# Kernel tuning notes

Hardware: AMD Instinct MI355X
Metric: run time of the kernel (lower is better)

## Reference

```python
import jax, jax.numpy as jnp
import numpy as np

N, E, C, R = 50000, 800000, 64, 8
H = 64  # MLP hidden width


def setup_inputs() -> dict:
    key = jax.random.key(0)
    ks = jax.random.split(key, 11)
    return {
        "node_features": jax.random.normal(ks[0], (N, 4 * C), jnp.float32),  # [0e: C] ++ [1o: C*3]
        "sph_harmonics": jax.random.normal(ks[1], (E, 4), jnp.float32),      # [Y_00, Y_1m (3)]
        "radial_basis": jax.random.normal(ks[2], (E, R), jnp.float32),
        "pre_W0": jax.random.normal(ks[3], (C, C), jnp.float32),
        "pre_W1": jax.random.normal(ks[4], (C, C), jnp.float32),
        "mlp_W1": jax.random.normal(ks[5], (R, H), jnp.float32) / np.sqrt(R),
        "mlp_W2": jax.random.normal(ks[6], (H, H), jnp.float32) / np.sqrt(H),
        "mlp_W3": jax.random.normal(ks[7], (H, 4 * C), jnp.float32) / np.sqrt(H),
        "post_W0": jax.random.normal(ks[8], (C, C), jnp.float32),
        "post_W1": jax.random.normal(ks[9], (C, C), jnp.float32),
        "edge_index": jax.random.randint(ks[10], (2, E), 0, N),  # row 0: receiver, row 1: sender
    }


def reference(node_features, sph_harmonics, radial_basis,
              pre_W0, pre_W1, mlp_W1, mlp_W2, mlp_W3, post_W0, post_W1,
              edge_index):
    n = node_features.shape[0]
    c = pre_W0.shape[0]
    inv_sqrt_c = 1.0 / jnp.sqrt(jnp.asarray(c, jnp.float32))
    INV_SQRT2 = 0.7071067811865476   # path normalization (2 paths per output irrep)
    INV_SQRT3 = 0.5773502691896258   # CG norm for 1o x 1o -> 0e (dot)

    # split flattened irreps: scalars [n, c], vectors [n, c, 3]
    x0 = node_features[:, :c]
    x1 = node_features[:, c:].reshape(n, c, 3)

    # pre_linear: per-irrep channel mixing (e3nn o3.Linear with 1/sqrt(fan_in))
    x0 = (x0 @ pre_W0) * inv_sqrt_c
    x1 = jnp.einsum('ncm,cd->ndm', x1, pre_W1) * inv_sqrt_c

    recv, send = edge_index[0], edge_index[1]

    # gather neighbour features (irregular access)
    xj0 = x0[send]            # [E, c]
    xj1 = x1[send]            # [E, c, 3]
    sh0 = sph_harmonics[:, :1]  # [E, 1]
    sh1 = sph_harmonics[:, 1:]  # [E, 3]

    # per-edge generated tensor-product weights: SiLU MLP, no bias, linear last layer
    h = jax.nn.silu(radial_basis @ mlp_W1)
    h = jax.nn.silu(h @ mlp_W2)
    w = h @ mlp_W3            # [E, 4c]
    w00, w110, w01, w10 = w[:, :c], w[:, c:2 * c], w[:, 2 * c:3 * c], w[:, 3 * c:]

    # channelwise CG tensor product with per-edge weights
    # 0e outputs: (0e x 0e) and (1o . 1o)/sqrt(3)
    m0 = (w00 * xj0 * sh0 + w110 * (jnp.einsum('ecm,em->ec', xj1, sh1) * INV_SQRT3)) * INV_SQRT2
    # 1o outputs: (0e x 1o) and (1o x 0e)
    m1 = (w01[:, :, None] * xj0[:, :, None] * sh1[:, None, :]
          + w10[:, :, None] * xj1 * sh0[:, :, None]) * INV_SQRT2   # [E, c, 3]

    # scatter-reduce (sum aggregation) into receiving nodes
    agg0 = jax.ops.segment_sum(m0, recv, num_segments=n)           # [n, c]
    agg1 = jax.ops.segment_sum(m1, recv, num_segments=n)           # [n, c, 3]

    # post_linear: per-irrep channel mixing
    y0 = (agg0 @ post_W0) * inv_sqrt_c
    y1 = jnp.einsum('ncm,cd->ndm', agg1, post_W1) * inv_sqrt_c

    # UnflattenIrreps -> [n, channels, sum(2l+1)] = [n, c, 4]
    return jnp.concatenate([y0[:, :, None], y1], axis=-1)
```

## Files before the change

kernel.cpp:

```cpp
#include <hip/hip_runtime.h>


#define FDIM 256
#define INV_SQRT2 0.7071067811865476f
#define INV_SQRT3 0.5773502691896258f

typedef __attribute__((ext_vector_type(8))) short s16x8;
typedef __attribute__((ext_vector_type(4))) float fx4;

__device__ __forceinline__ float silu_f(float x) { return x / (1.0f + __expf(-x)); }

__device__ __forceinline__ unsigned short f2bf(float x) {
    unsigned int u = __float_as_uint(x);
    u += 0x7FFFu + ((u >> 16) & 1u);
    return (unsigned short)(u >> 16);
}

__device__ __forceinline__ float bf2f(short v) {
    return __uint_as_float(((unsigned int)(unsigned short)v) << 16);
}

__device__ __forceinline__ int swz(int row) {
    return ((row & 7) ^ ((row >> 3) & 7)) << 4;
}

__global__ void __launch_bounds__(256) hist_pre_kernel(
    const int* __restrict__ ei, int* __restrict__ cnt, int E,
    const float* __restrict__ W1, const float* __restrict__ W2,
    const float* __restrict__ W3, float* __restrict__ W1t,
    unsigned short* __restrict__ W2bf, unsigned short* __restrict__ W3bf,
    const float* __restrict__ nf, const float* __restrict__ preW0,
    const float* __restrict__ preW1, unsigned short* __restrict__ xtb,
    int nNodes)
{
    int i = blockIdx.x * 256 + threadIdx.x;
    if (i < 512)  { int r = i >> 6, k = i & 63; W1t[k * 8 + r] = W1[i]; }
    if (i < 4096) { int j = i >> 6, k = i & 63; W2bf[i] = f2bf(W2[k * 64 + j]); }
    if (i < 16384) {
        int col = i >> 6, k = i & 63;
        int cb = col >> 5, r32 = col & 31, t = r32 >> 3, ci = r32 & 7;
        W3bf[i] = f2bf(W3[k * 256 + t * 64 + cb * 8 + ci]);
    }
    if (i < E) atomicAdd(&cnt[ei[i]], 1);

    const int lane = threadIdx.x & 63;
    const int wave = threadIdx.x >> 6;
    const int waveId = blockIdx.x * 4 + wave;
    const int nWaves = gridDim.x * 4;

    __shared__ __align__(16) float rowL[4][2][256];

    float w0r[64], w1r[64];
#pragma unroll
    for (int c = 0; c < 64; ++c) {
        w0r[c] = preW0[c * 64 + lane];
        w1r[c] = preW1[c * 64 + lane];
    }

    int n = waveId;
    if (n < nNodes) {
        float4 rv = *reinterpret_cast<const float4*>(nf + (size_t)n * FDIM + lane * 4);
        *reinterpret_cast<float4*>(&rowL[wave][0][lane * 4]) = rv;
    }
    int buf = 0;
    for (; n < nNodes; n += nWaves, buf ^= 1) {
        const int nn = n + nWaves;
        const bool hasNext = (nn < nNodes);
        float4 rvn;
        if (hasNext)
            rvn = *reinterpret_cast<const float4*>(nf + (size_t)nn * FDIM + lane * 4);

        asm volatile("s_waitcnt lgkmcnt(0)" ::: "memory");
        __builtin_amdgcn_sched_barrier(0);

        const float* __restrict__ row = rowL[wave][buf];
        float a0 = 0.f, a1 = 0.f, a2 = 0.f, a3 = 0.f;
#pragma unroll
        for (int c4 = 0; c4 < 16; ++c4) {
            fx4 x0 = *reinterpret_cast<const fx4*>(&row[c4 * 4]);
            fx4 xa = *reinterpret_cast<const fx4*>(&row[64 + c4 * 12]);
            fx4 xb = *reinterpret_cast<const fx4*>(&row[64 + c4 * 12 + 4]);
            fx4 xc = *reinterpret_cast<const fx4*>(&row[64 + c4 * 12 + 8]);
            const int c = c4 * 4;
            a0 = fmaf(x0[0], w0r[c + 0], a0);
            a1 = fmaf(xa[0], w1r[c + 0], a1);
            a2 = fmaf(xa[1], w1r[c + 0], a2);
            a3 = fmaf(xa[2], w1r[c + 0], a3);
            a0 = fmaf(x0[1], w0r[c + 1], a0);
            a1 = fmaf(xa[3], w1r[c + 1], a1);
            a2 = fmaf(xb[0], w1r[c + 1], a2);
            a3 = fmaf(xb[1], w1r[c + 1], a3);
            a0 = fmaf(x0[2], w0r[c + 2], a0);
            a1 = fmaf(xb[2], w1r[c + 2], a1);
            a2 = fmaf(xb[3], w1r[c + 2], a2);
            a3 = fmaf(xc[0], w1r[c + 2], a3);
            a0 = fmaf(x0[3], w0r[c + 3], a0);
            a1 = fmaf(xc[1], w1r[c + 3], a1);
            a2 = fmaf(xc[2], w1r[c + 3], a2);
            a3 = fmaf(xc[3], w1r[c + 3], a3);
        }
        __builtin_amdgcn_sched_barrier(0);

        unsigned short* o = xtb + (size_t)n * FDIM + (lane >> 3) * 32 + (lane & 7);
        o[0]  = f2bf(a0 * 0.125f);
        o[8]  = f2bf(a1 * 0.125f);
        o[16] = f2bf(a2 * 0.125f);
        o[24] = f2bf(a3 * 0.125f);

        if (hasNext)
            *reinterpret_cast<float4*>(&rowL[wave][buf ^ 1][lane * 4]) = rvn;
        __builtin_amdgcn_sched_barrier(0);
    }
}

__global__ void __launch_bounds__(1024) scan_kernel(
    const int* __restrict__ cnt, int* __restrict__ cursor, int nBins)
{
    __shared__ int part[1024];
    const int t = threadIdx.x;
    const int per = (nBins + 1023) / 1024;
    const int lo = t * per;
    const int hi = (lo + per < nBins) ? lo + per : nBins;

    int s = 0;
    for (int i = lo; i < hi; ++i) s += cnt[i];
    part[t] = s;
    __syncthreads();

    for (int off = 1; off < 1024; off <<= 1) {
        int v = part[t];
        int add = (t >= off) ? part[t - off] : 0;
        __syncthreads();
        part[t] = v + add;
        __syncthreads();
    }

    int run = part[t] - s;
    for (int i = lo; i < hi; ++i) {
        cursor[i] = run;
        run += cnt[i];
    }
}

__global__ void __launch_bounds__(256) scatter_perm_kernel(
    const int* __restrict__ ei, int* __restrict__ cursor,
    int* __restrict__ perm, int2* __restrict__ ers, int E)
{
    int i = blockIdx.x * 256 + threadIdx.x;
    if (i < E) {
        int r = ei[i];
        int p = atomicAdd(&cursor[r], 1);
        perm[p] = i;
        ers[p] = make_int2(r, ei[E + i]);
    }
}

__global__ void __launch_bounds__(256, 2) edge_kernel(
    const unsigned short* __restrict__ xtb, const float* __restrict__ sph,
    const float* __restrict__ rb, const int2* __restrict__ ers,
    const int* __restrict__ perm,
    const float* __restrict__ W1t, const unsigned short* __restrict__ W2bf,
    const unsigned short* __restrict__ W3bf, float* __restrict__ agg, int E)
{
    const int tid  = threadIdx.x;
    const int lane = tid & 63;
    const int wave = tid >> 6;
    const int eBase = blockIdx.x * 256 + wave * 64;
    const int idx = eBase + lane;
    const int idxSafe = (idx < E) ? idx : (E - 1);
    const int pe = perm[idxSafe];

    __shared__ __align__(16) char sbufAll[4][16384];
    __shared__ int recvL[4][64];
    char* const sbuf = sbufAll[wave];

    const float4 rq0 = *reinterpret_cast<const float4*>(rb + (size_t)pe * 8);
    const float4 rq1 = *reinterpret_cast<const float4*>(rb + (size_t)pe * 8 + 4);
    const float rbv[8] = {rq0.x, rq0.y, rq0.z, rq0.w, rq1.x, rq1.y, rq1.z, rq1.w};

    float h1[64];
#pragma unroll
    for (int k = 0; k < 64; ++k) {
        float acc = 0.f;
#pragma unroll
        for (int r = 0; r < 8; ++r) acc = fmaf(rbv[r], W1t[k * 8 + r], acc);
        h1[k] = silu_f(acc);
    }

#pragma unroll
    for (int q = 0; q < 8; ++q) {
        s16x8 v;
#pragma unroll
        for (int t = 0; t < 8; ++t) v[t] = (short)f2bf(h1[q * 8 + t]);
        *reinterpret_cast<s16x8*>(sbuf + lane * 128 + ((q * 16) ^ swz(lane))) = v;
    }

    const float4 shv = *reinterpret_cast<const float4*>(sph + (size_t)pe * 4);
    const float sh1a[3] = {shv.y, shv.z, shv.w};
    const int2 rs = ers[idxSafe];
    recvL[wave][lane] = rs.x;
    const unsigned short* __restrict__ xrow = xtb + (size_t)rs.y * FDIM;

    const int l15 = lane & 15;
    const int g4  = lane >> 4;

    s16x8 aH[4][2];
#pragma unroll
    for (int m = 0; m < 4; ++m)
#pragma unroll
        for (int kk = 0; kk < 2; ++kk) {
            int row = m * 16 + l15;
            aH[m][kk] = *reinterpret_cast<const s16x8*>(
                sbuf + row * 128 + ((kk * 64 + g4 * 16) ^ swz(row)));
        }

#pragma unroll
    for (int nh = 0; nh < 2; ++nh) {
        s16x8 bW2[2][2];
#pragma unroll
        for (int n2 = 0; n2 < 2; ++n2)
#pragma unroll
            for (int kk = 0; kk < 2; ++kk)
                bW2[n2][kk] = *reinterpret_cast<const s16x8*>(
                    W2bf + ((nh * 2 + n2) * 16 + l15) * 64 + kk * 32 + g4 * 8);

        fx4 acc2[4][2];
#pragma unroll
        for (int m = 0; m < 4; ++m)
#pragma unroll
            for (int n2 = 0; n2 < 2; ++n2) {
                fx4 z = {0.f, 0.f, 0.f, 0.f};
                acc2[m][n2] = z;
            }
#pragma unroll
        for (int kk = 0; kk < 2; ++kk)
#pragma unroll
            for (int m = 0; m < 4; ++m)
#pragma unroll
                for (int n2 = 0; n2 < 2; ++n2)
                    acc2[m][n2] = __builtin_amdgcn_mfma_f32_16x16x32_bf16(
                        aH[m][kk], bW2[n2][kk], acc2[m][n2], 0, 0, 0);

#pragma unroll
        for (int m = 0; m < 4; ++m)
#pragma unroll
            for (int n2 = 0; n2 < 2; ++n2)
#pragma unroll
                for (int r = 0; r < 4; ++r) {
                    int edge = m * 16 + g4 * 4 + r;
                    int j = (nh * 2 + n2) * 16 + l15;
                    *reinterpret_cast<unsigned short*>(
                        sbuf + edge * 128 + ((2 * j) ^ swz(edge))) =
                        f2bf(silu_f(acc2[m][n2][r]));
                }
    }

    s16x8 aH2[4][2];
#pragma unroll
    for (int m = 0; m < 4; ++m)
#pragma unroll
        for (int kk = 0; kk < 2; ++kk) {
            int row = m * 16 + l15;
            aH2[m][kk] = *reinterpret_cast<const s16x8*>(
                sbuf + row * 128 + ((kk * 64 + g4 * 16) ^ swz(row)));
        }

    const int jj  = lane & 31;
    const int sub = lane >> 5;
    const int base = sub * 32;
    float* const aggJJ = agg + jj;

    unsigned segmask = 0;
    {
        int rp = recvL[wave][base];
#pragma unroll
        for (int ep = 1; ep < 32; ++ep) {
            int r = recvL[wave][base + ep];
            if (r != rp) segmask |= (1u << ep);
            rp = r;
        }
    }

    for (int cbp = 0; cbp < 4; ++cbp) {
        s16x8 xjb2[8];
#pragma unroll
        for (int t = 0; t < 8; ++t)
            xjb2[t] = *reinterpret_cast<const s16x8*>(xrow + cbp * 64 + t * 8);

#pragma unroll
        for (int half = 0; half < 2; ++half) {
            const int cb = cbp * 2 + half;
            const s16x8* xjb = &xjb2[half * 4];

            s16x8 bW3[2][2];
#pragma unroll
            for (int n2 = 0; n2 < 2; ++n2)
#pragma unroll
                for (int kk = 0; kk < 2; ++kk)
                    bW3[n2][kk] = *reinterpret_cast<const s16x8*>(
                        W3bf + (cb * 32 + n2 * 16 + l15) * 64 + kk * 32 + g4 * 8);

            fx4 accw[4][2];
#pragma unroll
            for (int m = 0; m < 4; ++m)
#pragma unroll
                for (int n2 = 0; n2 < 2; ++n2) {
                    fx4 z = {0.f, 0.f, 0.f, 0.f};
                    accw[m][n2] = z;
                }
#pragma unroll
            for (int kk = 0; kk < 2; ++kk)
#pragma unroll
                for (int m = 0; m < 4; ++m)
#pragma unroll
                    for (int n2 = 0; n2 < 2; ++n2)
                        accw[m][n2] = __builtin_amdgcn_mfma_f32_16x16x32_bf16(
                            aH2[m][kk], bW3[n2][kk], accw[m][n2], 0, 0, 0);

#pragma unroll
            for (int m = 0; m < 4; ++m)
#pragma unroll
                for (int n2 = 0; n2 < 2; ++n2)
#pragma unroll
                    for (int r = 0; r < 4; ++r) {
                        int edge = m * 16 + g4 * 4 + r;
                        int c32 = n2 * 16 + l15;
                        *reinterpret_cast<float*>(
                            sbuf + edge * 128 + ((c32 * 4) ^ swz(edge))) = accw[m][n2][r];
                    }

            float wv[4][8];
#pragma unroll
            for (int t = 0; t < 4; ++t)
#pragma unroll
                for (int q = 0; q < 2; ++q) {
                    fx4 v = *reinterpret_cast<const fx4*>(
                        sbuf + lane * 128 + ((t * 32 + q * 16) ^ swz(lane)));
                    wv[t][q*4+0]=v.x; wv[t][q*4+1]=v.y; wv[t][q*4+2]=v.z; wv[t][q*4+3]=v.w;
                }

#pragma unroll
            for (int ci = 0; ci < 8; ++ci) {
                float x0v = bf2f(xjb[0][ci]);
                float x1a = bf2f(xjb[1][ci]);
                float x1b = bf2f(xjb[2][ci]);
                float x1c = bf2f(xjb[3][ci]);
                float dotv = (x1a * sh1a[0] + x1b * sh1a[1] + x1c * sh1a[2]) * INV_SQRT3;
                float m0 = (wv[0][ci] * x0v * shv.x + wv[1][ci] * dotv) * INV_SQRT2;
                float m1 = (wv[2][ci] * x0v * sh1a[0] + wv[3][ci] * x1a * shv.x) * INV_SQRT2;
                float m2 = (wv[2][ci] * x0v * sh1a[1] + wv[3][ci] * x1b * shv.x) * INV_SQRT2;
                float m3 = (wv[2][ci] * x0v * sh1a[2] + wv[3][ci] * x1c * shv.x) * INV_SQRT2;
                wv[0][ci] = m0; wv[1][ci] = m1; wv[2][ci] = m2; wv[3][ci] = m3;
            }
#pragma unroll
            for (int t = 0; t < 4; ++t)
#pragma unroll
                for (int q = 0; q < 2; ++q) {
                    fx4 v = {wv[t][q*4+0], wv[t][q*4+1], wv[t][q*4+2], wv[t][q*4+3]};
                    *reinterpret_cast<fx4*>(
                        sbuf + lane * 128 + ((t * 32 + q * 16) ^ swz(lane))) = v;
                }

            {
                int rprev = recvL[wave][base];
                float acc = 0.f;
                bool first = true;
#pragma unroll
                for (int ep = 0; ep < 32; ++ep) {
                    const int eL = base + ep;
                    float v = *reinterpret_cast<const float*>(
                        sbuf + eL * 128 + ((jj * 4) ^ swz(eL)));
                    if (eBase + eL >= E) v = 0.f;
                    if (segmask & (1u << ep)) {
                        float* dst = aggJJ + (size_t)rprev * FDIM + cb * 32;
                        if (first) atomicAdd(dst, acc);
                        else       *dst = acc;
                        first = false;
                        acc = 0.f;
                        rprev = recvL[wave][eL];
                    }
                    acc += v;
                }
                atomicAdd(aggJJ + (size_t)rprev * FDIM + cb * 32, acc);
            }
        }
    }
}

__global__ void __launch_bounds__(256) post_kernel(
    const float* __restrict__ agg, const float* __restrict__ W0,
    const float* __restrict__ W1, float* __restrict__ out, int nNodes)
{
    const int lane = threadIdx.x & 63;
    const int wave = threadIdx.x >> 6;
    const int waveId = blockIdx.x * 4 + wave;
    const int nWaves = gridDim.x * 4;

    __shared__ __align__(16) float rowL[4][2][256];

    float w0r[64], w1r[64];
#pragma unroll
    for (int c = 0; c < 64; ++c) {
        w0r[c] = W0[c * 64 + lane];
        w1r[c] = W1[c * 64 + lane];
    }

    int n = waveId;
    if (n < nNodes) {
        float4 rv = *reinterpret_cast<const float4*>(agg + (size_t)n * FDIM + lane * 4);
        *reinterpret_cast<float4*>(&rowL[wave][0][lane * 4]) = rv;
    }
    int buf = 0;
    for (; n < nNodes; n += nWaves, buf ^= 1) {
        const int nn = n + nWaves;
        const bool hasNext = (nn < nNodes);
        float4 rvn;
        if (hasNext)
            rvn = *reinterpret_cast<const float4*>(agg + (size_t)nn * FDIM + lane * 4);

        asm volatile("s_waitcnt lgkmcnt(0)" ::: "memory");
        __builtin_amdgcn_sched_barrier(0);

        const float* __restrict__ row = rowL[wave][buf];
        float a0 = 0.f, a1 = 0.f, a2 = 0.f, a3 = 0.f;
#pragma unroll
        for (int cb = 0; cb < 8; ++cb)
#pragma unroll
            for (int q = 0; q < 2; ++q) {
                const int c = cb * 8 + q * 4;
                fx4 v0 = *reinterpret_cast<const fx4*>(&row[cb*32 + q*4]);
                fx4 v1 = *reinterpret_cast<const fx4*>(&row[cb*32 + 8 + q*4]);
                fx4 v2 = *reinterpret_cast<const fx4*>(&row[cb*32 + 16 + q*4]);
                fx4 v3 = *reinterpret_cast<const fx4*>(&row[cb*32 + 24 + q*4]);
#pragma unroll
                for (int j = 0; j < 4; ++j) {
                    a0 = fmaf(v0[j], w0r[c + j], a0);
                    a1 = fmaf(v1[j], w1r[c + j], a1);
                    a2 = fmaf(v2[j], w1r[c + j], a2);
                    a3 = fmaf(v3[j], w1r[c + j], a3);
                }
            }
        __builtin_amdgcn_sched_barrier(0);

        float4 o4;
        o4.x = a0 * 0.125f;
        o4.y = a1 * 0.125f;
        o4.z = a2 * 0.125f;
        o4.w = a3 * 0.125f;
        *reinterpret_cast<float4*>(out + (size_t)n * FDIM + lane * 4) = o4;

        if (hasNext)
            *reinterpret_cast<float4*>(&rowL[wave][buf ^ 1][lane * 4]) = rvn;
        __builtin_amdgcn_sched_barrier(0);
    }
}

extern "C" void kernel_launch(void* const* d_in, const int* in_sizes, int n_in,
                              void* d_out, int out_size, void* d_ws, size_t ws_size,
                              hipStream_t stream) {
    const float* nf     = (const float*)d_in[0];
    const float* sph    = (const float*)d_in[1];
    const float* rb     = (const float*)d_in[2];
    const float* preW0  = (const float*)d_in[3];
    const float* preW1  = (const float*)d_in[4];
    const float* mlpW1  = (const float*)d_in[5];
    const float* mlpW2  = (const float*)d_in[6];
    const float* mlpW3  = (const float*)d_in[7];
    const float* postW0 = (const float*)d_in[8];
    const float* postW1 = (const float*)d_in[9];
    const int*   ei     = (const int*)d_in[10];

    const int N = in_sizes[0] / FDIM;
    const int E = in_sizes[1] / 4;

    float* agg = (float*)d_ws;
    int* cnt = (int*)(agg + (size_t)N * FDIM);
    unsigned short* xtb = (unsigned short*)(cnt + N);
    float* W1t = (float*)(xtb + (size_t)N * FDIM);
    unsigned short* W2bf = (unsigned short*)(W1t + 512);
    unsigned short* W3bf = W2bf + 4096;
    int* cursor = (int*)(W3bf + 16384);
    int* perm   = cursor + N;
    int2* ers   = (int2*)(perm + E);

    hipMemsetAsync(agg, 0, (size_t)N * FDIM * sizeof(float) + (size_t)N * sizeof(int),
                   stream);

    hist_pre_kernel<<<(E + 255) / 256, 256, 0, stream>>>(
        ei, cnt, E, mlpW1, mlpW2, mlpW3, W1t, W2bf, W3bf,
        nf, preW0, preW1, xtb, N);
    scan_kernel<<<1, 1024, 0, stream>>>(cnt, cursor, N);
    scatter_perm_kernel<<<(E + 255) / 256, 256, 0, stream>>>(ei, cursor, perm, ers, E);
    edge_kernel<<<(E + 255) / 256, 256, 0, stream>>>(
        xtb, sph, rb, ers, perm, W1t, W2bf, W3bf, agg, E);
    post_kernel<<<2048, 256, 0, stream>>>(agg, postW0, postW1, (float*)d_out, N);
}
```

Measured before the change: 490.6 us.

## Double-buffer neighbour feature gathers and alternate LDS halves across channel blocks

Moves the first sender-row gather ahead of the bf16 hidden-state LDS writes and prefetches the next channel-pair's gathered features into a second register buffer while the current pair is processed. This is meant to hide global-memory latency of the irregular gather behind MFMA and message compute. The two halves of each pair now use separate 8 KB halves of the per-wave LDS buffer, which reduces write-after-read hazards between consecutive blocks. The extra register buffer raises VGPR pressure, which could lower occupancy or cause spills.

```diff
diff --git a/kernel.cpp b/kernel.cpp
--- a/kernel.cpp
+++ b/kernel.cpp
@@ -187,19 +187,29 @@
         h1[k] = silu_f(acc);
     }
 
-#pragma unroll
-    for (int q = 0; q < 8; ++q) {
-        s16x8 v;
-#pragma unroll
-        for (int t = 0; t < 8; ++t) v[t] = (short)f2bf(h1[q * 8 + t]);
-        *reinterpret_cast<s16x8*>(sbuf + lane * 128 + ((q * 16) ^ swz(lane))) = v;
-    }
-
     const float4 shv = *reinterpret_cast<const float4*>(sph + (size_t)pe * 4);
     const float sh1a[3] = {shv.y, shv.z, shv.w};
     const int2 rs = ers[idxSafe];
     recvL[wave][lane] = rs.x;
     const unsigned short* __restrict__ xrow = xtb + (size_t)rs.y * FDIM;
+
+    s16x8 xjA[8], xjB[8];
+    auto issue_gather = [&](int cbp, s16x8* dst) {
+#pragma unroll
+        for (int t = 0; t < 8; ++t)
+            dst[t] = *reinterpret_cast<const s16x8*>(xrow + cbp * 64 + t * 8);
+    };
+
+    issue_gather(0, xjA);
+    __builtin_amdgcn_sched_barrier(0);
+
+#pragma unroll
+    for (int q = 0; q < 8; ++q) {
+        s16x8 v;
+#pragma unroll
+        for (int t = 0; t < 8; ++t) v[t] = (short)f2bf(h1[q * 8 + t]);
+        *reinterpret_cast<s16x8*>(sbuf + lane * 128 + ((q * 16) ^ swz(lane))) = v;
+    }
 
     const int l15 = lane & 15;
     const int g4  = lane >> 4;
@@ -281,16 +291,12 @@
         }
     }
 
-    for (int cbp = 0; cbp < 4; ++cbp) {
-        s16x8 xjb2[8];
-#pragma unroll
-        for (int t = 0; t < 8; ++t)
-            xjb2[t] = *reinterpret_cast<const s16x8*>(xrow + cbp * 64 + t * 8);
-
+    auto process_pair = [&](int cbp, const s16x8* xjb2) {
 #pragma unroll
         for (int half = 0; half < 2; ++half) {
             const int cb = cbp * 2 + half;
-            const s16x8* xjb = &xjb2[half * 4];
+            const s16x8* xjb = xjb2 + half * 4;
+            char* const sb = sbuf + half * 8192;
 
             s16x8 bW3[2][2];
 #pragma unroll
@@ -326,7 +332,7 @@
                         int edge = m * 16 + g4 * 4 + r;
                         int c32 = n2 * 16 + l15;
                         *reinterpret_cast<float*>(
-                            sbuf + edge * 128 + ((c32 * 4) ^ swz(edge))) = accw[m][n2][r];
+                            sb + edge * 128 + ((c32 * 4) ^ swz(edge))) = accw[m][n2][r];
                     }
 
             float wv[4][8];
@@ -335,7 +341,7 @@
 #pragma unroll
                 for (int q = 0; q < 2; ++q) {
                     fx4 v = *reinterpret_cast<const fx4*>(
-                        sbuf + lane * 128 + ((t * 32 + q * 16) ^ swz(lane)));
+                        sb + lane * 128 + ((t * 32 + q * 16) ^ swz(lane)));
                     wv[t][q*4+0]=v.x; wv[t][q*4+1]=v.y; wv[t][q*4+2]=v.z; wv[t][q*4+3]=v.w;
                 }
 
@@ -358,7 +364,7 @@
                 for (int q = 0; q < 2; ++q) {
                     fx4 v = {wv[t][q*4+0], wv[t][q*4+1], wv[t][q*4+2], wv[t][q*4+3]};
                     *reinterpret_cast<fx4*>(
-                        sbuf + lane * 128 + ((t * 32 + q * 16) ^ swz(lane))) = v;
+                        sb + lane * 128 + ((t * 32 + q * 16) ^ swz(lane))) = v;
                 }
 
             {
@@ -369,7 +375,7 @@
                 for (int ep = 0; ep < 32; ++ep) {
                     const int eL = base + ep;
                     float v = *reinterpret_cast<const float*>(
-                        sbuf + eL * 128 + ((jj * 4) ^ swz(eL)));
+                        sb + eL * 128 + ((jj * 4) ^ swz(eL)));
                     if (eBase + eL >= E) v = 0.f;
                     if (segmask & (1u << ep)) {
                         float* dst = aggJJ + (size_t)rprev * FDIM + cb * 32;
@@ -384,7 +390,18 @@
                 atomicAdd(aggJJ + (size_t)rprev * FDIM + cb * 32, acc);
             }
         }
-    }
+    };
+
+    issue_gather(1, xjB);
+    __builtin_amdgcn_sched_barrier(0);
+    process_pair(0, xjA);
+    issue_gather(2, xjA);
+    __builtin_amdgcn_sched_barrier(0);
+    process_pair(1, xjB);
+    issue_gather(3, xjB);
+    __builtin_amdgcn_sched_barrier(0);
+    process_pair(2, xjA);
+    process_pair(3, xjB);
 }
 
 __global__ void __launch_bounds__(256) post_kernel(
```

New measurement: 500.9 us. 2.1% more time.

## Compute post-linear channel mixing with bf16 MFMA over 64-node tiles

Applied to the files above, without the earlier changes.

Replaces the per-node scalar FMA post_kernel with a matrix-core version. Each wave handles 64 nodes, converts aggregated fp32 rows to bf16 and runs 16x16x32 bf16 MFMAs against post weights that hist_pre_kernel now pre-converts to bf16. The goal is to cut the FMA cost and the per-wave register-resident weight loads. In exchange it adds bf16 rounding of both the aggregates and the weights, and the output stores are strided scalar writes rather than coalesced float4 writes.

```diff
diff --git a/kernel.cpp b/kernel.cpp
--- a/kernel.cpp
+++ b/kernel.cpp
@@ -29,13 +29,20 @@
     const float* __restrict__ W1, const float* __restrict__ W2,
     const float* __restrict__ W3, float* __restrict__ W1t,
     unsigned short* __restrict__ W2bf, unsigned short* __restrict__ W3bf,
+    const float* __restrict__ postW0, const float* __restrict__ postW1,
+    unsigned short* __restrict__ W0pb, unsigned short* __restrict__ W1pb,
     const float* __restrict__ nf, const float* __restrict__ preW0,
     const float* __restrict__ preW1, unsigned short* __restrict__ xtb,
     int nNodes)
 {
     int i = blockIdx.x * 256 + threadIdx.x;
     if (i < 512)  { int r = i >> 6, k = i & 63; W1t[k * 8 + r] = W1[i]; }
-    if (i < 4096) { int j = i >> 6, k = i & 63; W2bf[i] = f2bf(W2[k * 64 + j]); }
+    if (i < 4096) {
+        int j = i >> 6, k = i & 63;
+        W2bf[i] = f2bf(W2[k * 64 + j]);
+        W0pb[i] = f2bf(postW0[k * 64 + j]);
+        W1pb[i] = f2bf(postW1[k * 64 + j]);
+    }
     if (i < 16384) {
         int col = i >> 6, k = i & 63;
         int cb = col >> 5, r32 = col & 31, t = r32 >> 3, ci = r32 & 7;
@@ -388,70 +395,78 @@
 }
 
 __global__ void __launch_bounds__(256) post_kernel(
-    const float* __restrict__ agg, const float* __restrict__ W0,
-    const float* __restrict__ W1, float* __restrict__ out, int nNodes)
+    const float* __restrict__ agg, const unsigned short* __restrict__ W0pb,
+    const unsigned short* __restrict__ W1pb, float* __restrict__ out, int nNodes)
 {
     const int lane = threadIdx.x & 63;
     const int wave = threadIdx.x >> 6;
     const int waveId = blockIdx.x * 4 + wave;
-    const int nWaves = gridDim.x * 4;
-
-    __shared__ __align__(16) float rowL[4][2][256];
-
-    float w0r[64], w1r[64];
-#pragma unroll
-    for (int c = 0; c < 64; ++c) {
-        w0r[c] = W0[c * 64 + lane];
-        w1r[c] = W1[c * 64 + lane];
-    }
-
-    int n = waveId;
-    if (n < nNodes) {
-        float4 rv = *reinterpret_cast<const float4*>(agg + (size_t)n * FDIM + lane * 4);
-        *reinterpret_cast<float4*>(&rowL[wave][0][lane * 4]) = rv;
-    }
-    int buf = 0;
-    for (; n < nNodes; n += nWaves, buf ^= 1) {
-        const int nn = n + nWaves;
-        const bool hasNext = (nn < nNodes);
-        float4 rvn;
-        if (hasNext)
-            rvn = *reinterpret_cast<const float4*>(agg + (size_t)nn * FDIM + lane * 4);
-
-        asm volatile("s_waitcnt lgkmcnt(0)" ::: "memory");
-        __builtin_amdgcn_sched_barrier(0);
-
-        const float* __restrict__ row = rowL[wave][buf];
-        float a0 = 0.f, a1 = 0.f, a2 = 0.f, a3 = 0.f;
-#pragma unroll
-        for (int cb = 0; cb < 8; ++cb)
-#pragma unroll
-            for (int q = 0; q < 2; ++q) {
-                const int c = cb * 8 + q * 4;
-                fx4 v0 = *reinterpret_cast<const fx4*>(&row[cb*32 + q*4]);
-                fx4 v1 = *reinterpret_cast<const fx4*>(&row[cb*32 + 8 + q*4]);
-                fx4 v2 = *reinterpret_cast<const fx4*>(&row[cb*32 + 16 + q*4]);
-                fx4 v3 = *reinterpret_cast<const fx4*>(&row[cb*32 + 24 + q*4]);
+    const int l15 = lane & 15;
+    const int g4  = lane >> 4;
+
+    const int nodeBase = waveId * 64;
+    if (nodeBase >= nNodes) return;
+
+    s16x8 b0[4][2], b1[4][2];
+#pragma unroll
+    for (int nt = 0; nt < 4; ++nt)
+#pragma unroll
+        for (int kk = 0; kk < 2; ++kk) {
+            b0[nt][kk] = *reinterpret_cast<const s16x8*>(
+                W0pb + (nt * 16 + l15) * 64 + kk * 32 + g4 * 8);
+            b1[nt][kk] = *reinterpret_cast<const s16x8*>(
+                W1pb + (nt * 16 + l15) * 64 + kk * 32 + g4 * 8);
+        }
+
+#pragma unroll
+    for (int t = 0; t < 4; ++t) {
+        s16x8 af[2][4];
+#pragma unroll
+        for (int kk = 0; kk < 2; ++kk)
+#pragma unroll
+            for (int m = 0; m < 4; ++m) {
+                int node = nodeBase + m * 16 + l15;
+                if (node >= nNodes) node = nNodes - 1;
+                const float* p = agg + (size_t)node * FDIM
+                               + (kk * 4 + g4) * 32 + t * 8;
+                fx4 u = *reinterpret_cast<const fx4*>(p);
+                fx4 v = *reinterpret_cast<const fx4*>(p + 4);
+                s16x8 a;
 #pragma unroll
                 for (int j = 0; j < 4; ++j) {
-                    a0 = fmaf(v0[j], w0r[c + j], a0);
-                    a1 = fmaf(v1[j], w1r[c + j], a1);
-                    a2 = fmaf(v2[j], w1r[c + j], a2);
-                    a3 = fmaf(v3[j], w1r[c + j], a3);
-                }
+                    a[j]     = (short)f2bf(u[j]);
+                    a[4 + j] = (short)f2bf(v[j]);
+                }
+                af[kk][m] = a;
             }
-        __builtin_amdgcn_sched_barrier(0);
-
-        float4 o4;
-        o4.x = a0 * 0.125f;
-        o4.y = a1 * 0.125f;
-        o4.z = a2 * 0.125f;
-        o4.w = a3 * 0.125f;
-        *reinterpret_cast<float4*>(out + (size_t)n * FDIM + lane * 4) = o4;
-
-        if (hasNext)
-            *reinterpret_cast<float4*>(&rowL[wave][buf ^ 1][lane * 4]) = rvn;
-        __builtin_amdgcn_sched_barrier(0);
+
+        const s16x8 (&bw)[4][2] = (t == 0) ? b0 : b1;
+
+#pragma unroll
+        for (int nt = 0; nt < 4; ++nt) {
+            fx4 acc[4];
+#pragma unroll
+            for (int m = 0; m < 4; ++m) {
+                fx4 z = {0.f, 0.f, 0.f, 0.f};
+                acc[m] = z;
+            }
+#pragma unroll
+            for (int kk = 0; kk < 2; ++kk)
+#pragma unroll
+                for (int m = 0; m < 4; ++m)
+                    acc[m] = __builtin_amdgcn_mfma_f32_16x16x32_bf16(
+                        af[kk][m], bw[nt][kk], acc[m], 0, 0, 0);
+
+#pragma unroll
+            for (int m = 0; m < 4; ++m)
+#pragma unroll
+                for (int r = 0; r < 4; ++r) {
+                    int node = nodeBase + m * 16 + g4 * 4 + r;
+                    if (node < nNodes)
+                        out[(size_t)node * FDIM + (nt * 16 + l15) * 4 + t] =
+                            acc[m][r] * 0.125f;
+                }
+        }
     }
 }
 
@@ -479,7 +494,9 @@
     float* W1t = (float*)(xtb + (size_t)N * FDIM);
     unsigned short* W2bf = (unsigned short*)(W1t + 512);
     unsigned short* W3bf = W2bf + 4096;
-    int* cursor = (int*)(W3bf + 16384);
+    unsigned short* W0pb = W3bf + 16384;
+    unsigned short* W1pb = W0pb + 4096;
+    int* cursor = (int*)(W1pb + 4096);
     int* perm   = cursor + N;
     int2* ers   = (int2*)(perm + E);
 
@@ -488,10 +505,12 @@
 
     hist_pre_kernel<<<(E + 255) / 256, 256, 0, stream>>>(
         ei, cnt, E, mlpW1, mlpW2, mlpW3, W1t, W2bf, W3bf,
+        postW0, postW1, W0pb, W1pb,
         nf, preW0, preW1, xtb, N);
     scan_kernel<<<1, 1024, 0, stream>>>(cnt, cursor, N);
     scatter_perm_kernel<<<(E + 255) / 256, 256, 0, stream>>>(ei, cursor, perm, ers, E);
     edge_kernel<<<(E + 255) / 256, 256, 0, stream>>>(
         xtb, sph, rb, ers, perm, W1t, W2bf, W3bf, agg, E);
-    post_kernel<<<2048, 256, 0, stream>>>(agg, postW0, postW1, (float*)d_out, N);
-}
+    post_kernel<<<(N + 255) / 256, 256, 0, stream>>>(
+        agg, W0pb, W1pb, (float*)d_out, N);
+}
```

Measured after the change: 502.7 us. 2.5% more time.
